# Performance work log

Hardware: AMD Instinct MI355X
Metric: run time of the kernel (lower is better)

The kernel has to match this reference:

```python
import jax, jax.numpy as jnp
import numpy as np

B, L, H, VOCAB, MAXLEN = 128, 256, 512, 32000, 256
DEPTH = 8  # L == 2**DEPTH complete binary trees

# Level offsets for internal nodes stored level-major (level 1 = just above leaves)
_OFF = np.zeros(DEPTH + 1, dtype=np.int64)
_s = 0
for _k in range(1, DEPTH + 1):
    _OFF[_k] = _s
    _s += L >> _k

# Post-order permutation of internal nodes (matches the iterative left-first
# traversal order in which the torch code appends hs)
def _post(k, j, acc):
    if k == 0:
        return
    _post(k - 1, 2 * j, acc)
    _post(k - 1, 2 * j + 1, acc)
    acc.append(int(_OFF[k]) + j)

_acc = []
_post(DEPTH, 0, _acc)
POST = np.asarray(_acc, dtype=np.int64)  # (L-1,)


def setup_inputs() -> dict:
    key = jax.random.key(0)
    ks = jax.random.split(key, 18)
    s = 1.0 / np.sqrt(H)
    d = {
        'word_idx': jax.random.randint(ks[0], (B, L), 0, VOCAB),
        'emb': jax.random.normal(ks[1], (VOCAB, H), jnp.float32) * s,
    }
    names = ['U_i_l', 'U_i_r', 'U_fl_l', 'U_fl_r', 'U_fr_l', 'U_fr_r',
             'U_o_l', 'U_o_r', 'U_c_l', 'U_c_r']
    for i, n in enumerate(names):
        d[n] = jax.random.normal(ks[2 + i], (H, H), jnp.float32) * s
    for i, n in enumerate(['b_i', 'b_fl', 'b_fr', 'b_o', 'b_c']):
        d[n] = jax.random.normal(ks[12 + i], (H,), jnp.float32) * 0.1
    return d


def reference(word_idx, emb, U_i_l, U_i_r, b_i, U_fl_l, U_fl_r, b_fl,
              U_fr_l, U_fr_r, b_fr, U_o_l, U_o_r, b_o, U_c_l, U_c_r, b_c):
    # Fuse the 5 gate projections per side into one GEMM: (5H, H)
    Wl = jnp.concatenate([U_i_l, U_fl_l, U_fr_l, U_o_l, U_c_l], axis=0)
    Wr = jnp.concatenate([U_i_r, U_fl_r, U_fr_r, U_o_r, U_c_r], axis=0)
    b = jnp.concatenate([b_i, b_fl, b_fr, b_o, b_c], axis=0)

    def combine(hl, hr, cl, cr):
        # hl/hr: (B, n, H); torch does U @ h with h (H,1) -> h @ U.T batched
        z = jnp.einsum('bnh,gh->bng', hl, Wl) + jnp.einsum('bnh,gh->bng', hr, Wr) + b
        i, fl, fr, o, c = jnp.split(z, 5, axis=-1)
        c_phr = jax.nn.sigmoid(i) * jnp.tanh(c) \
            + jax.nn.sigmoid(fl) * cl + jax.nn.sigmoid(fr) * cr
        h_phr = jax.nn.sigmoid(o) * jnp.tanh(c_phr)
        return h_phr, c_phr

    # Leaves: h = embedding row, c = 0.5 (torch: ones - 0.5)
    h = emb[word_idx]                      # (B, L, H)
    c = jnp.full((B, L, H), 0.5, emb.dtype)

    internal_hs = []
    for _ in range(DEPTH):  # level-synchronous bottom-up combine
        h, c = combine(h[:, 0::2], h[:, 1::2], c[:, 0::2], c[:, 1::2])
        internal_hs.append(h)

    H_int = jnp.concatenate(internal_hs, axis=1)  # (B, L-1, H), level-major
    post = jnp.asarray(POST)
    # torch bug faithfully reproduced: hs[0] is prepended, then all hs appended
    out = jnp.concatenate([H_int[:, post[:1]], H_int[:, post]], axis=1)  # (B, MAXLEN, H)

    forest_h = jnp.swapaxes(h, 0, 1)  # (1, B, H)
    forest_c = jnp.swapaxes(c, 0, 1)  # (1, B, H)
    return out, (forest_h, forest_c)
```

## Files before the change

### kernel.cpp

```cpp
#include <hip/hip_runtime.h>

#define NB 128
#define NL 256
#define NH 512
#define NMAX 256

typedef __attribute__((ext_vector_type(8))) short s8v;
typedef __attribute__((ext_vector_type(4))) float f4v;

struct Params {
  const int* widx;
  const float* bias[5];
  const unsigned short* wbf;
  const unsigned short* embbf;
  const unsigned short* hcprev;
  unsigned short* hcout;
  unsigned short* part;
  float* out;
  float* fh;
  float* fc;
};

struct PrepParams {
  const float* u[10];
  const float* emb;
  unsigned short* wdst;
  unsigned short* edst;
};

__device__ __forceinline__ float bf2f(unsigned short u) {
  union { unsigned int i; float f; } v;
  v.i = ((unsigned int)u) << 16;
  return v.f;
}
__device__ __forceinline__ unsigned short f2bf(float f) {
  union { float f; unsigned int i; } v;
  v.f = f;
  unsigned int x = v.i;
  x += 0x7fffu + ((x >> 16) & 1u);
  return (unsigned short)(x >> 16);
}
__device__ __forceinline__ s8v pack8(f4v a, f4v b) {
  s8v r;
  r[0] = (short)f2bf(a[0]); r[1] = (short)f2bf(a[1]);
  r[2] = (short)f2bf(a[2]); r[3] = (short)f2bf(a[3]);
  r[4] = (short)f2bf(b[0]); r[5] = (short)f2bf(b[1]);
  r[6] = (short)f2bf(b[2]); r[7] = (short)f2bf(b[3]);
  return r;
}
__device__ __forceinline__ float sigf(float x) {
  return 1.f / (1.f + __expf(-x));
}
__device__ __forceinline__ void glds16(const void* g, void* l) {
  __builtin_amdgcn_global_load_lds(
      (const __attribute__((address_space(1))) unsigned int*)g,
      (__attribute__((address_space(3))) unsigned int*)l, 16, 0, 0);
}

__global__ __launch_bounds__(256) void prep_cvt(PrepParams pp) {
  int gid = blockIdx.x * 256 + threadIdx.x;
  const float* s;
  unsigned short* d;
  if (gid < 327680) {
    int mat = gid >> 15, off = (gid & 32767) * 8;
    s = pp.u[mat] + off;
    d = pp.wdst + (size_t)mat * NH * NH + off;
  } else {
    size_t off = (size_t)(gid - 327680) * 8;
    s = pp.emb + off;
    d = pp.edst + off;
  }
  f4v x0 = *(const f4v*)s;
  f4v x1 = *(const f4v*)(s + 4);
  *(s8v*)d = pack8(x0, x1);
}


template<int LEVEL, int BM, int KS>
__global__ __launch_bounds__(BM * 2, 2)
void lstm_level(Params p) {
  constexpr int NK = NL >> LEVEL;
  constexpr int LOGNK = 8 - LEVEL;
  constexpr int NKP = NL >> (LEVEL - 1);
  constexpr int M = NB * NK;
  constexpr int W = BM / 32;
  constexpr int ASUB = BM * 64;
  constexpr int BUFSZ = ASUB + 20480;
  constexpr int NT = 32 / KS;
  __shared__ __align__(16) unsigned char lds[2 * BUFSZ];

  const int tid = threadIdx.x;
  const int wid = tid >> 6;
  const int lane = tid & 63;
  const int lhi = lane >> 4, llo = lane & 15;
  const int mh = (BM == 256) ? (wid & 1) : 0;
  const int q  = (BM == 256) ? (wid >> 1) : wid;
  const int bm = blockIdx.x, ht = blockIdx.y;
  const int ks = (KS > 1) ? blockIdx.z : 0;
  const int t0 = ks * NT;

  const unsigned short* abase = (LEVEL == 1) ? p.embbf : p.hcprev;

  int aOffL[2], aOffR[2];
#pragma unroll
  for (int ii = 0; ii < 2; ++ii) {
    int gi = ii * W + wid;
    int ar = gi * 16 + (lane >> 2);
    int ck = (lane & 3) ^ ((ar >> 1) & 3);
    int am = bm * BM + ar; if (am > M - 1) am = M - 1;
    int b = am >> LOGNK, j = am & (NK - 1);
    if constexpr (LEVEL == 1) {
      aOffL[ii] = p.widx[b * NL + 2 * j] * NH + ck * 8;
      aOffR[ii] = p.widx[b * NL + 2 * j + 1] * NH + ck * 8;
    } else {
      int base = (b * NKP + 2 * j) * (2 * NH);
      aOffL[ii] = base + ck * 8;
      aOffR[ii] = base + 2 * NH + ck * 8;
    }
  }

  constexpr int BI = (20 + W - 1) / W;
  int bOff[BI];
#pragma unroll
  for (int ii = 0; ii < BI; ++ii) {
    int gi = ii * W + wid;
    if (gi < 20) {
      int r = gi * 16 + (lane >> 2);
      int gg = gi >> 2;
      int ck = (lane & 3) ^ ((r >> 1) & 3);
      bOff[ii] = ((2 * gg) * NH + (ht * 64 + (r & 63))) * NH + ck * 8;
    } else bOff[ii] = 0;
  }

  auto do_stage = [&](int buf, int tt) {
    unsigned char* base = lds + buf * BUFSZ;
    const int kw = (tt & 15) * 32;
    const int* ao = (tt < 16) ? aOffL : aOffR;
#pragma unroll
    for (int ii = 0; ii < 2; ++ii)
      glds16(abase + ao[ii] + kw, base + (ii * W + wid) * 1024);
    const size_t wsel = (size_t)(tt >> 4) * NH * NH;
#pragma unroll
    for (int ii = 0; ii < BI; ++ii) {
      int gi = ii * W + wid;
      if (gi < 20)
        glds16(p.wbf + wsel + bOff[ii] + kw, base + ASUB + gi * 1024);
    }
  };

  int aoff[8], boff[5];
#pragma unroll
  for (int fm = 0; fm < 8; ++fm) {
    int r = mh * 128 + fm * 16 + llo;
    aoff[fm] = r * 64 + ((lhi ^ ((r >> 1) & 3)) << 4);
  }
#pragma unroll
  for (int g = 0; g < 5; ++g) {
    int r = g * 64 + q * 16 + llo;
    boff[g] = ASUB + r * 64 + ((lhi ^ ((r >> 1) & 3)) << 4);
  }

  f4v acc[8][5];
#pragma unroll
  for (int fm = 0; fm < 8; ++fm)
#pragma unroll
    for (int g = 0; g < 5; ++g)
      acc[fm][g] = (f4v){0.f, 0.f, 0.f, 0.f};

  auto compute = [&](int buf) {
    const unsigned char* base = lds + buf * BUFSZ;
    s8v af[8], bv[5];
#pragma unroll
    for (int fm = 0; fm < 8; ++fm) af[fm] = *(const s8v*)(base + aoff[fm]);
#pragma unroll
    for (int g = 0; g < 5; ++g)  bv[g] = *(const s8v*)(base + boff[g]);
    __builtin_amdgcn_s_setprio(1);
#pragma unroll
    for (int fm = 0; fm < 8; ++fm)
#pragma unroll
      for (int g = 0; g < 5; ++g)
        acc[fm][g] = __builtin_amdgcn_mfma_f32_16x16x32_bf16(
            af[fm], bv[g], acc[fm][g], 0, 0, 0);
    __builtin_amdgcn_s_setprio(0);
  };

  do_stage(0, t0);
  __syncthreads();
  for (int t = 0; t < NT; ++t) {
    const int cur = t & 1;
    if (t + 1 < NT) do_stage(cur ^ 1, t0 + t + 1);
    compute(cur);
    __syncthreads();
  }

  const int hdl = q * 16 + llo;

  if constexpr (KS > 1) {
#pragma unroll
    for (int fm = 0; fm < 8; ++fm) {
#pragma unroll
      for (int jj = 0; jj < 4; ++jj) {
        int m = bm * BM + mh * 128 + fm * 16 + lhi * 4 + jj;
        size_t base = (((size_t)(ks * M + m) * 8 + ht) * 5) * 64;
#pragma unroll
        for (int g = 0; g < 5; ++g)
          p.part[base + g * 64 + hdl] = f2bf(acc[fm][g][jj]);
      }
    }
  } else {
    const int hd = ht * 64 + hdl;
    float bb[5];
#pragma unroll
    for (int g = 0; g < 5; ++g) bb[g] = p.bias[g][hd];

#pragma unroll
    for (int fm = 0; fm < 8; ++fm) {
#pragma unroll
      for (int jj = 0; jj < 4; ++jj) {
        int m = bm * BM + mh * 128 + fm * 16 + lhi * 4 + jj;
        if (m < M) {
          int b = m >> LOGNK, j = m & (NK - 1);
          float zi  = acc[fm][0][jj] + bb[0];
          float zfl = acc[fm][1][jj] + bb[1];
          float zfr = acc[fm][2][jj] + bb[2];
          float zo  = acc[fm][3][jj] + bb[3];
          float zc  = acc[fm][4][jj] + bb[4];
          float cl = 0.5f, cr = 0.5f;
          if constexpr (LEVEL > 1) {
            const unsigned short* cb =
                p.hcprev + ((size_t)b * NKP + 2 * j) * (2 * NH) + NH;
            cl = bf2f(cb[hd]);
            cr = bf2f(cb[2 * NH + hd]);
          }
          float cnew = sigf(zi) * tanhf(zc) + sigf(zfl) * cl + sigf(zfr) * cr;
          float hnew = sigf(zo) * tanhf(cnew);
          unsigned short* orow = p.hcout + ((size_t)b * NK + j) * (2 * NH);
          orow[hd] = f2bf(hnew);
          orow[NH + hd] = f2bf(cnew);
          int colout = (((j + 1) << LEVEL) - 2 - __popc(j)) + 1;
          p.out[((size_t)b * NMAX + colout) * NH + hd] = hnew;
          if (LEVEL == 1 && j == 0) p.out[(size_t)b * NMAX * NH + hd] = hnew;
          if constexpr (LEVEL == 8) { p.fh[b * NH + hd] = hnew; p.fc[b * NH + hd] = cnew; }
        }
      }
    }
  }
}

template<int LEVEL, int KS>
__global__ __launch_bounds__(256)
void lstm_combine(Params p) {
  constexpr int NK = NL >> LEVEL;
  constexpr int LOGNK = 8 - LEVEL;
  constexpr int NKP = NL >> (LEVEL - 1);
  constexpr int M = NB * NK;
  int t = blockIdx.x * 256 + threadIdx.x;
  int m = t >> 9, hd = t & 511;
  int ht = hd >> 6, hdl = hd & 63;
  int b = m >> LOGNK, j = m & (NK - 1);

  float z[5];
#pragma unroll
  for (int g = 0; g < 5; ++g) z[g] = p.bias[g][hd];
  for (int ks = 0; ks < KS; ++ks) {
    size_t base = (((size_t)(ks * M + m) * 8 + ht) * 5) * 64;
#pragma unroll
    for (int g = 0; g < 5; ++g) z[g] += bf2f(p.part[base + g * 64 + hdl]);
  }
  const unsigned short* cb = p.hcprev + ((size_t)b * NKP + 2 * j) * (2 * NH) + NH;
  float cl = bf2f(cb[hd]);
  float cr = bf2f(cb[2 * NH + hd]);
  float cnew = sigf(z[0]) * tanhf(z[4]) + sigf(z[1]) * cl + sigf(z[2]) * cr;
  float hnew = sigf(z[3]) * tanhf(cnew);
  unsigned short* orow = p.hcout + ((size_t)b * NK + j) * (2 * NH);
  orow[hd] = f2bf(hnew);
  orow[NH + hd] = f2bf(cnew);
  int colout = (((j + 1) << LEVEL) - 2 - __popc(j)) + 1;
  p.out[((size_t)b * NMAX + colout) * NH + hd] = hnew;
  if constexpr (LEVEL == 8) { p.fh[b * NH + hd] = hnew; p.fc[b * NH + hd] = cnew; }
}

extern "C" void kernel_launch(void* const* d_in, const int* in_sizes, int n_in,
                              void* d_out, int out_size, void* d_ws, size_t ws_size,
                              hipStream_t stream) {
  unsigned short* wbf = (unsigned short*)d_ws;
  unsigned short* R1  = wbf + (size_t)10 * NH * NH;
  unsigned short* R2  = R1 + 16777216;

  PrepParams pp;
  for (int i = 0; i < 10; ++i) pp.u[i] = (const float*)d_in[2 + i];
  pp.emb  = (const float*)d_in[1];
  pp.wdst = wbf;
  pp.edst = R1;

  Params p;
  p.widx = (const int*)d_in[0];
  for (int g = 0; g < 5; ++g) p.bias[g] = (const float*)d_in[12 + g];
  p.wbf   = wbf;
  p.embbf = R1;
  p.part  = nullptr;
  p.out   = (float*)d_out;
  p.fh    = p.out + (size_t)NB * NMAX * NH;
  p.fc    = p.fh + NB * NH;

  prep_cvt<<<dim3(9280), dim3(256), 0, stream>>>(pp);

  unsigned short* lvlout[9];
  for (int k = 1; k <= 8; ++k) lvlout[k] = (k & 1) ? R2 : R1;

  p.hcprev = nullptr;     p.hcout = lvlout[1];
  lstm_level<1, 256, 1><<<dim3(64, 8), dim3(512), 0, stream>>>(p);
  p.hcprev = lvlout[1];   p.hcout = lvlout[2];
  lstm_level<2, 128, 1><<<dim3(64, 8), dim3(256), 0, stream>>>(p);
  p.hcprev = lvlout[2];   p.hcout = lvlout[3];
  lstm_level<3, 128, 1><<<dim3(32, 8), dim3(256), 0, stream>>>(p);

  p.hcprev = lvlout[3];   p.hcout = lvlout[4];
  p.part   = lvlout[3] + 6 * 1024 * 1024;
  lstm_level<4, 128, 2><<<dim3(16, 8, 2), dim3(256), 0, stream>>>(p);
  lstm_combine<4, 2><<<dim3(4096), dim3(256), 0, stream>>>(p);

  p.hcprev = lvlout[4];   p.hcout = lvlout[5];
  p.part   = lvlout[4] + 4 * 1024 * 1024;
  lstm_level<5, 128, 4><<<dim3(8, 8, 4), dim3(256), 0, stream>>>(p);
  lstm_combine<5, 4><<<dim3(2048), dim3(256), 0, stream>>>(p);

  p.hcprev = lvlout[5];   p.hcout = lvlout[6];
  p.part   = lvlout[5] + 4 * 1024 * 1024;
  lstm_level<6, 128, 4><<<dim3(4, 8, 4), dim3(256), 0, stream>>>(p);
  lstm_combine<6, 4><<<dim3(1024), dim3(256), 0, stream>>>(p);

  p.hcprev = lvlout[6];   p.hcout = lvlout[7];
  p.part   = lvlout[6] + 4 * 1024 * 1024;
  lstm_level<7, 128, 8><<<dim3(2, 8, 8), dim3(256), 0, stream>>>(p);
  lstm_combine<7, 8><<<dim3(512), dim3(256), 0, stream>>>(p);

  p.hcprev = lvlout[7];   p.hcout = lvlout[8];
  p.part   = lvlout[7] + 4 * 1024 * 1024;
  lstm_level<8, 128, 8><<<dim3(1, 8, 8), dim3(256), 0, stream>>>(p);
  lstm_combine<8, 8><<<dim3(256), dim3(256), 0, stream>>>(p);
}
```

Before: 309.4 us.

## Fuse levels 3-8 into one persistent kernel with grid barriers

Replaces the per-level GEMM and split-K combine launches for levels 3 through 8 with a single persistent 256-block kernel. Levels are separated by a software grid barrier built on atomics. Split-K factors are raised so every level keeps all 256 blocks busy (up to 32 K-slices at the root). This removes roughly a dozen kernel launch gaps and raises parallelism at the small top levels. In exchange it adds barrier spin cost and depends on all 256 blocks being co-resident, which carries a deadlock risk if they are not.

```diff
diff --git a/kernel.cpp b/kernel.cpp
--- a/kernel.cpp
+++ b/kernel.cpp
@@ -15,10 +15,20 @@
   const unsigned short* embbf;
   const unsigned short* hcprev;
   unsigned short* hcout;
-  unsigned short* part;
   float* out;
   float* fh;
   float* fc;
+};
+
+struct TailP {
+  const float* bias[5];
+  const unsigned short* wbf;
+  unsigned short* hc[9];
+  unsigned short* part[9];
+  float* out;
+  float* fh;
+  float* fc;
+  int* bar;
 };
 
 struct PrepParams {
@@ -55,6 +65,23 @@
   __builtin_amdgcn_global_load_lds(
       (const __attribute__((address_space(1))) unsigned int*)g,
       (__attribute__((address_space(3))) unsigned int*)l, 16, 0, 0);
+}
+
+__device__ __forceinline__ void gbar(int* bar) {
+  __threadfence();
+  __syncthreads();
+  if (threadIdx.x == 0) {
+    int g = __hip_atomic_load(bar + 1, __ATOMIC_RELAXED, __HIP_MEMORY_SCOPE_AGENT);
+    if (__hip_atomic_fetch_add(bar, 1, __ATOMIC_ACQ_REL, __HIP_MEMORY_SCOPE_AGENT) == 255) {
+      __hip_atomic_store(bar, 0, __ATOMIC_RELAXED, __HIP_MEMORY_SCOPE_AGENT);
+      __hip_atomic_fetch_add(bar + 1, 1, __ATOMIC_ACQ_REL, __HIP_MEMORY_SCOPE_AGENT);
+    } else {
+      while (__hip_atomic_load(bar + 1, __ATOMIC_ACQUIRE, __HIP_MEMORY_SCOPE_AGENT) == g)
+        __builtin_amdgcn_s_sleep(8);
+    }
+  }
+  __syncthreads();
+  __threadfence();
 }
 
 __global__ __launch_bounds__(256) void prep_cvt(PrepParams pp) {
@@ -76,7 +103,7 @@
 }
 
 
-template<int LEVEL, int BM, int KS>
+template<int LEVEL, int BM>
 __global__ __launch_bounds__(BM * 2, 2)
 void lstm_level(Params p) {
   constexpr int NK = NL >> LEVEL;
@@ -86,7 +113,6 @@
   constexpr int W = BM / 32;
   constexpr int ASUB = BM * 64;
   constexpr int BUFSZ = ASUB + 20480;
-  constexpr int NT = 32 / KS;
   __shared__ __align__(16) unsigned char lds[2 * BUFSZ];
 
   const int tid = threadIdx.x;
@@ -96,8 +122,6 @@
   const int mh = (BM == 256) ? (wid & 1) : 0;
   const int q  = (BM == 256) ? (wid >> 1) : wid;
   const int bm = blockIdx.x, ht = blockIdx.y;
-  const int ks = (KS > 1) ? blockIdx.z : 0;
-  const int t0 = ks * NT;
 
   const unsigned short* abase = (LEVEL == 1) ? p.embbf : p.hcprev;
 
@@ -184,6 +208,149 @@
     __builtin_amdgcn_s_setprio(0);
   };
 
+  do_stage(0, 0);
+  __syncthreads();
+  for (int t = 0; t < 32; ++t) {
+    const int cur = t & 1;
+    if (t + 1 < 32) do_stage(cur ^ 1, t + 1);
+    compute(cur);
+    __syncthreads();
+  }
+
+  const int hd = ht * 64 + q * 16 + llo;
+  float bb[5];
+#pragma unroll
+  for (int g = 0; g < 5; ++g) bb[g] = p.bias[g][hd];
+
+#pragma unroll
+  for (int fm = 0; fm < 8; ++fm) {
+#pragma unroll
+    for (int jj = 0; jj < 4; ++jj) {
+      int m = bm * BM + mh * 128 + fm * 16 + lhi * 4 + jj;
+      if (m < M) {
+        int b = m >> LOGNK, j = m & (NK - 1);
+        float zi  = acc[fm][0][jj] + bb[0];
+        float zfl = acc[fm][1][jj] + bb[1];
+        float zfr = acc[fm][2][jj] + bb[2];
+        float zo  = acc[fm][3][jj] + bb[3];
+        float zc  = acc[fm][4][jj] + bb[4];
+        float cl = 0.5f, cr = 0.5f;
+        if constexpr (LEVEL > 1) {
+          const unsigned short* cb =
+              p.hcprev + ((size_t)b * NKP + 2 * j) * (2 * NH) + NH;
+          cl = bf2f(cb[hd]);
+          cr = bf2f(cb[2 * NH + hd]);
+        }
+        float cnew = sigf(zi) * tanhf(zc) + sigf(zfl) * cl + sigf(zfr) * cr;
+        float hnew = sigf(zo) * tanhf(cnew);
+        unsigned short* orow = p.hcout + ((size_t)b * NK + j) * (2 * NH);
+        orow[hd] = f2bf(hnew);
+        orow[NH + hd] = f2bf(cnew);
+        int colout = (((j + 1) << LEVEL) - 2 - __popc(j)) + 1;
+        p.out[((size_t)b * NMAX + colout) * NH + hd] = hnew;
+        if (LEVEL == 1 && j == 0) p.out[(size_t)b * NMAX * NH + hd] = hnew;
+      }
+    }
+  }
+}
+
+template<int LEVEL, int KS>
+__device__ void tail_gemm(const TailP& tp, unsigned char* lds, int bid) {
+  constexpr int NK = NL >> LEVEL;
+  constexpr int LOGNK = 8 - LEVEL;
+  constexpr int NKP = NL >> (LEVEL - 1);
+  constexpr int M = NB * NK;
+  constexpr int BMX = M / 128;
+  constexpr int NT = 32 / KS;
+  constexpr int ASUB = 8192;
+  constexpr int BUFSZ = 28672;
+  const int bm = bid % BMX;
+  const int ht = (bid / BMX) & 7;
+  const int ks = bid / (BMX * 8);
+  const int t0 = ks * NT;
+  const int tid = threadIdx.x;
+  const int wid = tid >> 6, lane = tid & 63;
+  const int lhi = lane >> 4, llo = lane & 15;
+  const int q = wid;
+  const unsigned short* hcprev = tp.hc[LEVEL - 1];
+
+  int aOffL[2], aOffR[2];
+#pragma unroll
+  for (int ii = 0; ii < 2; ++ii) {
+    int gi = ii * 4 + wid;
+    int ar = gi * 16 + (lane >> 2);
+    int ck = (lane & 3) ^ ((ar >> 1) & 3);
+    int am = bm * 128 + ar;
+    int b = am >> LOGNK, j = am & (NK - 1);
+    int base = (b * NKP + 2 * j) * (2 * NH);
+    aOffL[ii] = base + ck * 8;
+    aOffR[ii] = base + 2 * NH + ck * 8;
+  }
+
+  int bOff[5];
+#pragma unroll
+  for (int ii = 0; ii < 5; ++ii) {
+    int gi = ii * 4 + wid;
+    if (gi < 20) {
+      int r = gi * 16 + (lane >> 2);
+      int gg = gi >> 2;
+      int ck = (lane & 3) ^ ((r >> 1) & 3);
+      bOff[ii] = ((2 * gg) * NH + (ht * 64 + (r & 63))) * NH + ck * 8;
+    } else bOff[ii] = 0;
+  }
+
+  auto do_stage = [&](int buf, int tt) {
+    unsigned char* base = lds + buf * BUFSZ;
+    const int kw = (tt & 15) * 32;
+    const int* ao = (tt < 16) ? aOffL : aOffR;
+#pragma unroll
+    for (int ii = 0; ii < 2; ++ii)
+      glds16(hcprev + ao[ii] + kw, base + (ii * 4 + wid) * 1024);
+    const size_t wsel = (size_t)(tt >> 4) * NH * NH;
+#pragma unroll
+    for (int ii = 0; ii < 5; ++ii) {
+      int gi = ii * 4 + wid;
+      if (gi < 20)
+        glds16(tp.wbf + wsel + bOff[ii] + kw, base + ASUB + gi * 1024);
+    }
+  };
+
+  int aoff[8], boff[5];
+#pragma unroll
+  for (int fm = 0; fm < 8; ++fm) {
+    int r = fm * 16 + llo;
+    aoff[fm] = r * 64 + ((lhi ^ ((r >> 1) & 3)) << 4);
+  }
+#pragma unroll
+  for (int g = 0; g < 5; ++g) {
+    int r = g * 64 + q * 16 + llo;
+    boff[g] = ASUB + r * 64 + ((lhi ^ ((r >> 1) & 3)) << 4);
+  }
+
+  f4v acc[8][5];
+#pragma unroll
+  for (int fm = 0; fm < 8; ++fm)
+#pragma unroll
+    for (int g = 0; g < 5; ++g)
+      acc[fm][g] = (f4v){0.f, 0.f, 0.f, 0.f};
+
+  auto compute = [&](int buf) {
+    const unsigned char* base = lds + buf * BUFSZ;
+    s8v af[8], bv[5];
+#pragma unroll
+    for (int fm = 0; fm < 8; ++fm) af[fm] = *(const s8v*)(base + aoff[fm]);
+#pragma unroll
+    for (int g = 0; g < 5; ++g)  bv[g] = *(const s8v*)(base + boff[g]);
+    __builtin_amdgcn_s_setprio(1);
+#pragma unroll
+    for (int fm = 0; fm < 8; ++fm)
+#pragma unroll
+      for (int g = 0; g < 5; ++g)
+        acc[fm][g] = __builtin_amdgcn_mfma_f32_16x16x32_bf16(
+            af[fm], bv[g], acc[fm][g], 0, 0, 0);
+    __builtin_amdgcn_s_setprio(0);
+  };
+
   do_stage(0, t0);
   __syncthreads();
   for (int t = 0; t < NT; ++t) {
@@ -194,90 +361,108 @@
   }
 
   const int hdl = q * 16 + llo;
-
   if constexpr (KS > 1) {
 #pragma unroll
     for (int fm = 0; fm < 8; ++fm) {
 #pragma unroll
       for (int jj = 0; jj < 4; ++jj) {
-        int m = bm * BM + mh * 128 + fm * 16 + lhi * 4 + jj;
+        int m = bm * 128 + fm * 16 + lhi * 4 + jj;
         size_t base = (((size_t)(ks * M + m) * 8 + ht) * 5) * 64;
 #pragma unroll
         for (int g = 0; g < 5; ++g)
-          p.part[base + g * 64 + hdl] = f2bf(acc[fm][g][jj]);
+          tp.part[LEVEL][base + g * 64 + hdl] = f2bf(acc[fm][g][jj]);
       }
     }
   } else {
     const int hd = ht * 64 + hdl;
     float bb[5];
 #pragma unroll
-    for (int g = 0; g < 5; ++g) bb[g] = p.bias[g][hd];
-
+    for (int g = 0; g < 5; ++g) bb[g] = tp.bias[g][hd];
 #pragma unroll
     for (int fm = 0; fm < 8; ++fm) {
 #pragma unroll
       for (int jj = 0; jj < 4; ++jj) {
-        int m = bm * BM + mh * 128 + fm * 16 + lhi * 4 + jj;
-        if (m < M) {
-          int b = m >> LOGNK, j = m & (NK - 1);
-          float zi  = acc[fm][0][jj] + bb[0];
-          float zfl = acc[fm][1][jj] + bb[1];
-          float zfr = acc[fm][2][jj] + bb[2];
-          float zo  = acc[fm][3][jj] + bb[3];
-          float zc  = acc[fm][4][jj] + bb[4];
-          float cl = 0.5f, cr = 0.5f;
-          if constexpr (LEVEL > 1) {
-            const unsigned short* cb =
-                p.hcprev + ((size_t)b * NKP + 2 * j) * (2 * NH) + NH;
-            cl = bf2f(cb[hd]);
-            cr = bf2f(cb[2 * NH + hd]);
-          }
-          float cnew = sigf(zi) * tanhf(zc) + sigf(zfl) * cl + sigf(zfr) * cr;
-          float hnew = sigf(zo) * tanhf(cnew);
-          unsigned short* orow = p.hcout + ((size_t)b * NK + j) * (2 * NH);
-          orow[hd] = f2bf(hnew);
-          orow[NH + hd] = f2bf(cnew);
-          int colout = (((j + 1) << LEVEL) - 2 - __popc(j)) + 1;
-          p.out[((size_t)b * NMAX + colout) * NH + hd] = hnew;
-          if (LEVEL == 1 && j == 0) p.out[(size_t)b * NMAX * NH + hd] = hnew;
-          if constexpr (LEVEL == 8) { p.fh[b * NH + hd] = hnew; p.fc[b * NH + hd] = cnew; }
-        }
+        int m = bm * 128 + fm * 16 + lhi * 4 + jj;
+        int b = m >> LOGNK, j = m & (NK - 1);
+        float zi  = acc[fm][0][jj] + bb[0];
+        float zfl = acc[fm][1][jj] + bb[1];
+        float zfr = acc[fm][2][jj] + bb[2];
+        float zo  = acc[fm][3][jj] + bb[3];
+        float zc  = acc[fm][4][jj] + bb[4];
+        const unsigned short* cb = hcprev + ((size_t)b * NKP + 2 * j) * (2 * NH) + NH;
+        float cl = bf2f(cb[hd]);
+        float cr = bf2f(cb[2 * NH + hd]);
+        float cnew = sigf(zi) * tanhf(zc) + sigf(zfl) * cl + sigf(zfr) * cr;
+        float hnew = sigf(zo) * tanhf(cnew);
+        unsigned short* orow = tp.hc[LEVEL] + ((size_t)b * NK + j) * (2 * NH);
+        orow[hd] = f2bf(hnew);
+        orow[NH + hd] = f2bf(cnew);
+        int colout = (((j + 1) << LEVEL) - 2 - __popc(j)) + 1;
+        tp.out[((size_t)b * NMAX + colout) * NH + hd] = hnew;
       }
     }
   }
 }
 
 template<int LEVEL, int KS>
-__global__ __launch_bounds__(256)
-void lstm_combine(Params p) {
+__device__ void tail_combine(const TailP& tp, int bid) {
   constexpr int NK = NL >> LEVEL;
   constexpr int LOGNK = 8 - LEVEL;
   constexpr int NKP = NL >> (LEVEL - 1);
   constexpr int M = NB * NK;
-  int t = blockIdx.x * 256 + threadIdx.x;
-  int m = t >> 9, hd = t & 511;
-  int ht = hd >> 6, hdl = hd & 63;
-  int b = m >> LOGNK, j = m & (NK - 1);
-
-  float z[5];
-#pragma unroll
-  for (int g = 0; g < 5; ++g) z[g] = p.bias[g][hd];
-  for (int ks = 0; ks < KS; ++ks) {
-    size_t base = (((size_t)(ks * M + m) * 8 + ht) * 5) * 64;
-#pragma unroll
-    for (int g = 0; g < 5; ++g) z[g] += bf2f(p.part[base + g * 64 + hdl]);
-  }
-  const unsigned short* cb = p.hcprev + ((size_t)b * NKP + 2 * j) * (2 * NH) + NH;
-  float cl = bf2f(cb[hd]);
-  float cr = bf2f(cb[2 * NH + hd]);
-  float cnew = sigf(z[0]) * tanhf(z[4]) + sigf(z[1]) * cl + sigf(z[2]) * cr;
-  float hnew = sigf(z[3]) * tanhf(cnew);
-  unsigned short* orow = p.hcout + ((size_t)b * NK + j) * (2 * NH);
-  orow[hd] = f2bf(hnew);
-  orow[NH + hd] = f2bf(cnew);
-  int colout = (((j + 1) << LEVEL) - 2 - __popc(j)) + 1;
-  p.out[((size_t)b * NMAX + colout) * NH + hd] = hnew;
-  if constexpr (LEVEL == 8) { p.fh[b * NH + hd] = hnew; p.fc[b * NH + hd] = cnew; }
+  const unsigned short* part = tp.part[LEVEL];
+  const unsigned short* hcprev = tp.hc[LEVEL - 1];
+  for (int t = bid * 256 + threadIdx.x; t < M * 512; t += 256 * 256) {
+    int m = t >> 9, hd = t & 511;
+    int ht = hd >> 6, hdl = hd & 63;
+    int b = m >> LOGNK, j = m & (NK - 1);
+    float z[5];
+#pragma unroll
+    for (int g = 0; g < 5; ++g) z[g] = tp.bias[g][hd];
+    for (int ks = 0; ks < KS; ++ks) {
+      size_t base = (((size_t)(ks * M + m) * 8 + ht) * 5) * 64;
+#pragma unroll
+      for (int g = 0; g < 5; ++g) z[g] += bf2f(part[base + g * 64 + hdl]);
+    }
+    const unsigned short* cb = hcprev + ((size_t)b * NKP + 2 * j) * (2 * NH) + NH;
+    float cl = bf2f(cb[hd]);
+    float cr = bf2f(cb[2 * NH + hd]);
+    float cnew = sigf(z[0]) * tanhf(z[4]) + sigf(z[1]) * cl + sigf(z[2]) * cr;
+    float hnew = sigf(z[3]) * tanhf(cnew);
+    unsigned short* orow = tp.hc[LEVEL] + ((size_t)b * NK + j) * (2 * NH);
+    orow[hd] = f2bf(hnew);
+    orow[NH + hd] = f2bf(cnew);
+    int colout = (((j + 1) << LEVEL) - 2 - __popc(j)) + 1;
+    tp.out[((size_t)b * NMAX + colout) * NH + hd] = hnew;
+    if constexpr (LEVEL == 8) { tp.fh[b * NH + hd] = hnew; tp.fc[b * NH + hd] = cnew; }
+  }
+}
+
+__global__ __launch_bounds__(256, 2)
+void lstm_tail(TailP tp) {
+  __shared__ __align__(16) unsigned char lds[57344];
+  const int bid = blockIdx.x;
+  tail_gemm<3, 1>(tp, lds, bid);
+  gbar(tp.bar);
+  tail_gemm<4, 2>(tp, lds, bid);
+  gbar(tp.bar);
+  tail_combine<4, 2>(tp, bid);
+  gbar(tp.bar);
+  tail_gemm<5, 4>(tp, lds, bid);
+  gbar(tp.bar);
+  tail_combine<5, 4>(tp, bid);
+  gbar(tp.bar);
+  tail_gemm<6, 8>(tp, lds, bid);
+  gbar(tp.bar);
+  tail_combine<6, 8>(tp, bid);
+  gbar(tp.bar);
+  tail_gemm<7, 16>(tp, lds, bid);
+  gbar(tp.bar);
+  tail_combine<7, 16>(tp, bid);
+  gbar(tp.bar);
+  tail_gemm<8, 32>(tp, lds, bid);
+  gbar(tp.bar);
+  tail_combine<8, 32>(tp, bid);
 }
 
 extern "C" void kernel_launch(void* const* d_in, const int* in_sizes, int n_in,
@@ -298,7 +483,6 @@
   for (int g = 0; g < 5; ++g) p.bias[g] = (const float*)d_in[12 + g];
   p.wbf   = wbf;
   p.embbf = R1;
-  p.part  = nullptr;
   p.out   = (float*)d_out;
   p.fh    = p.out + (size_t)NB * NMAX * NH;
   p.fc    = p.fh + NB * NH;
@@ -309,34 +493,27 @@
   for (int k = 1; k <= 8; ++k) lvlout[k] = (k & 1) ? R2 : R1;
 
   p.hcprev = nullptr;     p.hcout = lvlout[1];
-  lstm_level<1, 256, 1><<<dim3(64, 8), dim3(512), 0, stream>>>(p);
+  lstm_level<1, 256><<<dim3(64, 8), dim3(512), 0, stream>>>(p);
   p.hcprev = lvlout[1];   p.hcout = lvlout[2];
-  lstm_level<2, 128, 1><<<dim3(64, 8), dim3(256), 0, stream>>>(p);
-  p.hcprev = lvlout[2];   p.hcout = lvlout[3];
-  lstm_level<3, 128, 1><<<dim3(32, 8), dim3(256), 0, stream>>>(p);
-
-  p.hcprev = lvlout[3];   p.hcout = lvlout[4];
-  p.part   = lvlout[3] + 6 * 1024 * 1024;
-  lstm_level<4, 128, 2><<<dim3(16, 8, 2), dim3(256), 0, stream>>>(p);
-  lstm_combine<4, 2><<<dim3(4096), dim3(256), 0, stream>>>(p);
-
-  p.hcprev = lvlout[4];   p.hcout = lvlout[5];
-  p.part   = lvlout[4] + 4 * 1024 * 1024;
-  lstm_level<5, 128, 4><<<dim3(8, 8, 4), dim3(256), 0, stream>>>(p);
-  lstm_combine<5, 4><<<dim3(2048), dim3(256), 0, stream>>>(p);
-
-  p.hcprev = lvlout[5];   p.hcout = lvlout[6];
-  p.part   = lvlout[5] + 4 * 1024 * 1024;
-  lstm_level<6, 128, 4><<<dim3(4, 8, 4), dim3(256), 0, stream>>>(p);
-  lstm_combine<6, 4><<<dim3(1024), dim3(256), 0, stream>>>(p);
-
-  p.hcprev = lvlout[6];   p.hcout = lvlout[7];
-  p.part   = lvlout[6] + 4 * 1024 * 1024;
-  lstm_level<7, 128, 8><<<dim3(2, 8, 8), dim3(256), 0, stream>>>(p);
-  lstm_combine<7, 8><<<dim3(512), dim3(256), 0, stream>>>(p);
-
-  p.hcprev = lvlout[7];   p.hcout = lvlout[8];
-  p.part   = lvlout[7] + 4 * 1024 * 1024;
-  lstm_level<8, 128, 8><<<dim3(1, 8, 8), dim3(256), 0, stream>>>(p);
-  lstm_combine<8, 8><<<dim3(256), dim3(256), 0, stream>>>(p);
-}
+  lstm_level<2, 128><<<dim3(64, 8), dim3(256), 0, stream>>>(p);
+
+  int* bar = (int*)(R1 + 16000000);
+  hipMemsetAsync(bar, 0, 64, stream);
+
+  TailP tp;
+  for (int g = 0; g < 5; ++g) tp.bias[g] = p.bias[g];
+  tp.wbf = wbf;
+  for (int k = 1; k <= 8; ++k) tp.hc[k] = lvlout[k];
+  tp.hc[0] = nullptr;
+  for (int k = 0; k < 9; ++k) tp.part[k] = nullptr;
+  tp.part[4] = R2 + (size_t)6 * 1024 * 1024;
+  tp.part[5] = R1 + (size_t)4 * 1024 * 1024;
+  tp.part[6] = R2 + (size_t)4 * 1024 * 1024;
+  tp.part[7] = R1 + (size_t)4 * 1024 * 1024;
+  tp.part[8] = R2 + (size_t)4 * 1024 * 1024;
+  tp.out = p.out;
+  tp.fh  = p.fh;
+  tp.fc  = p.fc;
+  tp.bar = bar;
+  lstm_tail<<<dim3(256), dim3(256), 0, stream>>>(tp);
+}
```

Result: slower. 1.070 ms (+245.9%).

## Process multiple M tiles per block in level-1 GEMM and prefetch next tile during epilogue

Applied to the files above, without the earlier changes.

Adds a TILES template parameter so each workgroup loops over several consecutive M tiles, reusing setup such as B-offsets and bias loads. While one tile's gate epilogue runs, the first K-stage of the next tile is already being loaded into LDS, overlapping the epilogue with memory traffic. Only level 1 uses TILES=2, which halves its grid from 512 to 256 workgroups. That trades parallelism and wave count for less per-block setup and some overlap.

```diff
diff --git a/kernel.cpp b/kernel.cpp
--- a/kernel.cpp
+++ b/kernel.cpp
@@ -76,7 +76,7 @@
 }
 
 
-template<int LEVEL, int BM, int KS>
+template<int LEVEL, int BM, int KS, int TILES>
 __global__ __launch_bounds__(BM * 2, 2)
 void lstm_level(Params p) {
   constexpr int NK = NL >> LEVEL;
@@ -95,29 +95,31 @@
   const int lhi = lane >> 4, llo = lane & 15;
   const int mh = (BM == 256) ? (wid & 1) : 0;
   const int q  = (BM == 256) ? (wid >> 1) : wid;
-  const int bm = blockIdx.x, ht = blockIdx.y;
+  const int ht = blockIdx.y;
   const int ks = (KS > 1) ? blockIdx.z : 0;
   const int t0 = ks * NT;
 
   const unsigned short* abase = (LEVEL == 1) ? p.embbf : p.hcprev;
 
   int aOffL[2], aOffR[2];
-#pragma unroll
-  for (int ii = 0; ii < 2; ++ii) {
-    int gi = ii * W + wid;
-    int ar = gi * 16 + (lane >> 2);
-    int ck = (lane & 3) ^ ((ar >> 1) & 3);
-    int am = bm * BM + ar; if (am > M - 1) am = M - 1;
-    int b = am >> LOGNK, j = am & (NK - 1);
-    if constexpr (LEVEL == 1) {
-      aOffL[ii] = p.widx[b * NL + 2 * j] * NH + ck * 8;
-      aOffR[ii] = p.widx[b * NL + 2 * j + 1] * NH + ck * 8;
-    } else {
-      int base = (b * NKP + 2 * j) * (2 * NH);
-      aOffL[ii] = base + ck * 8;
-      aOffR[ii] = base + 2 * NH + ck * 8;
-    }
-  }
+  auto computeA = [&](int bm) {
+#pragma unroll
+    for (int ii = 0; ii < 2; ++ii) {
+      int gi = ii * W + wid;
+      int ar = gi * 16 + (lane >> 2);
+      int ck = (lane & 3) ^ ((ar >> 1) & 3);
+      int am = bm * BM + ar; if (am > M - 1) am = M - 1;
+      int b = am >> LOGNK, j = am & (NK - 1);
+      if constexpr (LEVEL == 1) {
+        aOffL[ii] = p.widx[b * NL + 2 * j] * NH + ck * 8;
+        aOffR[ii] = p.widx[b * NL + 2 * j + 1] * NH + ck * 8;
+      } else {
+        int base = (b * NKP + 2 * j) * (2 * NH);
+        aOffL[ii] = base + ck * 8;
+        aOffR[ii] = base + 2 * NH + ck * 8;
+      }
+    }
+  };
 
   constexpr int BI = (20 + W - 1) / W;
   int bOff[BI];
@@ -161,11 +163,6 @@
   }
 
   f4v acc[8][5];
-#pragma unroll
-  for (int fm = 0; fm < 8; ++fm)
-#pragma unroll
-    for (int g = 0; g < 5; ++g)
-      acc[fm][g] = (f4v){0.f, 0.f, 0.f, 0.f};
 
   auto compute = [&](int buf) {
     const unsigned char* base = lds + buf * BUFSZ;
@@ -184,63 +181,79 @@
     __builtin_amdgcn_s_setprio(0);
   };
 
+  const int hdl = q * 16 + llo;
+  float bb[5];
+#pragma unroll
+  for (int g = 0; g < 5; ++g) bb[g] = p.bias[g][ht * 64 + hdl];
+
+  int bmCur = blockIdx.x * TILES;
+  computeA(bmCur);
   do_stage(0, t0);
-  __syncthreads();
-  for (int t = 0; t < NT; ++t) {
-    const int cur = t & 1;
-    if (t + 1 < NT) do_stage(cur ^ 1, t0 + t + 1);
-    compute(cur);
+
+#pragma unroll
+  for (int it = 0; it < TILES; ++it) {
+#pragma unroll
+    for (int fm = 0; fm < 8; ++fm)
+#pragma unroll
+      for (int g = 0; g < 5; ++g)
+        acc[fm][g] = (f4v){0.f, 0.f, 0.f, 0.f};
     __syncthreads();
-  }
-
-  const int hdl = q * 16 + llo;
-
-  if constexpr (KS > 1) {
-#pragma unroll
-    for (int fm = 0; fm < 8; ++fm) {
-#pragma unroll
-      for (int jj = 0; jj < 4; ++jj) {
-        int m = bm * BM + mh * 128 + fm * 16 + lhi * 4 + jj;
-        size_t base = (((size_t)(ks * M + m) * 8 + ht) * 5) * 64;
-#pragma unroll
-        for (int g = 0; g < 5; ++g)
-          p.part[base + g * 64 + hdl] = f2bf(acc[fm][g][jj]);
+    for (int t = 0; t < NT; ++t) {
+      const int cur = t & 1;
+      if (t + 1 < NT) do_stage(cur ^ 1, t0 + t + 1);
+      compute(cur);
+      if (t + 1 < NT) __syncthreads();
+    }
+    const int bmOut = bmCur;
+    if (it + 1 < TILES) {
+      bmCur = blockIdx.x * TILES + it + 1;
+      computeA(bmCur);
+      do_stage(0, t0);
+    }
+
+    if constexpr (KS > 1) {
+#pragma unroll
+      for (int fm = 0; fm < 8; ++fm) {
+#pragma unroll
+        for (int jj = 0; jj < 4; ++jj) {
+          int m = bmOut * BM + mh * 128 + fm * 16 + lhi * 4 + jj;
+          size_t base = (((size_t)(ks * M + m) * 8 + ht) * 5) * 64;
+#pragma unroll
+          for (int g = 0; g < 5; ++g)
+            p.part[base + g * 64 + hdl] = f2bf(acc[fm][g][jj]);
+        }
       }
-    }
-  } else {
-    const int hd = ht * 64 + hdl;
-    float bb[5];
-#pragma unroll
-    for (int g = 0; g < 5; ++g) bb[g] = p.bias[g][hd];
-
-#pragma unroll
-    for (int fm = 0; fm < 8; ++fm) {
-#pragma unroll
-      for (int jj = 0; jj < 4; ++jj) {
-        int m = bm * BM + mh * 128 + fm * 16 + lhi * 4 + jj;
-        if (m < M) {
-          int b = m >> LOGNK, j = m & (NK - 1);
-          float zi  = acc[fm][0][jj] + bb[0];
-          float zfl = acc[fm][1][jj] + bb[1];
-          float zfr = acc[fm][2][jj] + bb[2];
-          float zo  = acc[fm][3][jj] + bb[3];
-          float zc  = acc[fm][4][jj] + bb[4];
-          float cl = 0.5f, cr = 0.5f;
-          if constexpr (LEVEL > 1) {
-            const unsigned short* cb =
-                p.hcprev + ((size_t)b * NKP + 2 * j) * (2 * NH) + NH;
-            cl = bf2f(cb[hd]);
-            cr = bf2f(cb[2 * NH + hd]);
+    } else {
+      const int hd = ht * 64 + hdl;
+#pragma unroll
+      for (int fm = 0; fm < 8; ++fm) {
+#pragma unroll
+        for (int jj = 0; jj < 4; ++jj) {
+          int m = bmOut * BM + mh * 128 + fm * 16 + lhi * 4 + jj;
+          if (m < M) {
+            int b = m >> LOGNK, j = m & (NK - 1);
+            float zi  = acc[fm][0][jj] + bb[0];
+            float zfl = acc[fm][1][jj] + bb[1];
+            float zfr = acc[fm][2][jj] + bb[2];
+            float zo  = acc[fm][3][jj] + bb[3];
+            float zc  = acc[fm][4][jj] + bb[4];
+            float cl = 0.5f, cr = 0.5f;
+            if constexpr (LEVEL > 1) {
+              const unsigned short* cb =
+                  p.hcprev + ((size_t)b * NKP + 2 * j) * (2 * NH) + NH;
+              cl = bf2f(cb[hd]);
+              cr = bf2f(cb[2 * NH + hd]);
+            }
+            float cnew = sigf(zi) * tanhf(zc) + sigf(zfl) * cl + sigf(zfr) * cr;
+            float hnew = sigf(zo) * tanhf(cnew);
+            unsigned short* orow = p.hcout + ((size_t)b * NK + j) * (2 * NH);
+            orow[hd] = f2bf(hnew);
+            orow[NH + hd] = f2bf(cnew);
+            int colout = (((j + 1) << LEVEL) - 2 - __popc(j)) + 1;
+            p.out[((size_t)b * NMAX + colout) * NH + hd] = hnew;
+            if (LEVEL == 1 && j == 0) p.out[(size_t)b * NMAX * NH + hd] = hnew;
+            if constexpr (LEVEL == 8) { p.fh[b * NH + hd] = hnew; p.fc[b * NH + hd] = cnew; }
           }
-          float cnew = sigf(zi) * tanhf(zc) + sigf(zfl) * cl + sigf(zfr) * cr;
-          float hnew = sigf(zo) * tanhf(cnew);
-          unsigned short* orow = p.hcout + ((size_t)b * NK + j) * (2 * NH);
-          orow[hd] = f2bf(hnew);
-          orow[NH + hd] = f2bf(cnew);
-          int colout = (((j + 1) << LEVEL) - 2 - __popc(j)) + 1;
-          p.out[((size_t)b * NMAX + colout) * NH + hd] = hnew;
-          if (LEVEL == 1 && j == 0) p.out[(size_t)b * NMAX * NH + hd] = hnew;
-          if constexpr (LEVEL == 8) { p.fh[b * NH + hd] = hnew; p.fc[b * NH + hd] = cnew; }
         }
       }
     }
@@ -309,34 +322,34 @@
   for (int k = 1; k <= 8; ++k) lvlout[k] = (k & 1) ? R2 : R1;
 
   p.hcprev = nullptr;     p.hcout = lvlout[1];
-  lstm_level<1, 256, 1><<<dim3(64, 8), dim3(512), 0, stream>>>(p);
+  lstm_level<1, 256, 1, 2><<<dim3(32, 8), dim3(512), 0, stream>>>(p);
   p.hcprev = lvlout[1];   p.hcout = lvlout[2];
-  lstm_level<2, 128, 1><<<dim3(64, 8), dim3(256), 0, stream>>>(p);
+  lstm_level<2, 128, 1, 1><<<dim3(64, 8), dim3(256), 0, stream>>>(p);
   p.hcprev = lvlout[2];   p.hcout = lvlout[3];
-  lstm_level<3, 128, 1><<<dim3(32, 8), dim3(256), 0, stream>>>(p);
+  lstm_level<3, 128, 1, 1><<<dim3(32, 8), dim3(256), 0, stream>>>(p);
 
   p.hcprev = lvlout[3];   p.hcout = lvlout[4];
   p.part   = lvlout[3] + 6 * 1024 * 1024;
-  lstm_level<4, 128, 2><<<dim3(16, 8, 2), dim3(256), 0, stream>>>(p);
+  lstm_level<4, 128, 2, 1><<<dim3(16, 8, 2), dim3(256), 0, stream>>>(p);
   lstm_combine<4, 2><<<dim3(4096), dim3(256), 0, stream>>>(p);
 
   p.hcprev = lvlout[4];   p.hcout = lvlout[5];
   p.part   = lvlout[4] + 4 * 1024 * 1024;
-  lstm_level<5, 128, 4><<<dim3(8, 8, 4), dim3(256), 0, stream>>>(p);
+  lstm_level<5, 128, 4, 1><<<dim3(8, 8, 4), dim3(256), 0, stream>>>(p);
   lstm_combine<5, 4><<<dim3(2048), dim3(256), 0, stream>>>(p);
 
   p.hcprev = lvlout[5];   p.hcout = lvlout[6];
   p.part   = lvlout[5] + 4 * 1024 * 1024;
-  lstm_level<6, 128, 4><<<dim3(4, 8, 4), dim3(256), 0, stream>>>(p);
+  lstm_level<6, 128, 4, 1><<<dim3(4, 8, 4), dim3(256), 0, stream>>>(p);
   lstm_combine<6, 4><<<dim3(1024), dim3(256), 0, stream>>>(p);
 
   p.hcprev = lvlout[6];   p.hcout = lvlout[7];
   p.part   = lvlout[6] + 4 * 1024 * 1024;
-  lstm_level<7, 128, 8><<<dim3(2, 8, 8), dim3(256), 0, stream>>>(p);
+  lstm_level<7, 128, 8, 1><<<dim3(2, 8, 8), dim3(256), 0, stream>>>(p);
   lstm_combine<7, 8><<<dim3(512), dim3(256), 0, stream>>>(p);
 
   p.hcprev = lvlout[7];   p.hcout = lvlout[8];
   p.part   = lvlout[7] + 4 * 1024 * 1024;
-  lstm_level<8, 128, 8><<<dim3(1, 8, 8), dim3(256), 0, stream>>>(p);
+  lstm_level<8, 128, 8, 1><<<dim3(1, 8, 8), dim3(256), 0, stream>>>(p);
   lstm_combine<8, 8><<<dim3(256), dim3(256), 0, stream>>>(p);
 }
```

New measurement: 302.8 us, median of 2. 1.02x faster.
